# Kernel optimization log

Measured on AMD Instinct MI355X. Metric: run time of the kernel, lower is better.

The kernel has to match this reference:

```python
import jax, jax.numpy as jnp
import numpy as np

N_HEAD = 12
N_EMBD = 768
HEAD_DIM = N_EMBD // N_HEAD


def setup_inputs() -> dict:
    key = jax.random.key(0)
    k1, k2, k3, k4, k5 = jax.random.split(key, 5)
    B, T, C = 1, 4096, N_EMBD
    s = 0.02
    return {
        "x": jax.random.normal(k1, (B, T, C), dtype=jnp.float32),
        "W_qkv": jax.random.normal(k2, (C, 3 * C), dtype=jnp.float32) * s,
        "b_qkv": jnp.zeros((3 * C,), dtype=jnp.float32),
        "W_out": jax.random.normal(k3, (C, C), dtype=jnp.float32) * s,
        "b_out": jnp.zeros((C,), dtype=jnp.float32),
    }


def reference(x, W_qkv, b_qkv, W_out, b_out):
    B, T, C = x.shape
    H, D = N_HEAD, HEAD_DIM
    qkv = x @ W_qkv + b_qkv                       # (B, T, 3C)
    qkv = qkv.reshape(B, T, 3, H, D)
    q = jnp.transpose(qkv[:, :, 0], (0, 2, 1, 3))  # (B, H, T, D)
    k = jnp.transpose(qkv[:, :, 1], (0, 2, 1, 3))
    v = jnp.transpose(qkv[:, :, 2], (0, 2, 1, 3))
    scores = jnp.einsum("bhqd,bhkd->bhqk", q, k) / jnp.sqrt(jnp.float32(D))
    causal = jnp.tril(jnp.ones((T, T), dtype=bool))
    scores = jnp.where(causal[None, None], scores, -jnp.inf)
    weights = jax.nn.softmax(scores, axis=-1)     # (B, H, T, T)
    out = jnp.einsum("bhqk,bhkd->bhqd", weights, v)
    out = jnp.transpose(out, (0, 2, 1, 3)).reshape(B, T, C)
    return out @ W_out + b_out
```

## Files before the change

### kernel.cpp

```cpp
#include <hip/hip_runtime.h>
#include <hip/hip_bf16.h>
#include <stdint.h>

#define T_SEQ 4096
#define C_EMB 768
#define C3    2304
#define CQK   1536
#define NH    12
#define HD    64

typedef __attribute__((ext_vector_type(8))) short short8;
typedef __attribute__((ext_vector_type(4))) short short4v;
typedef __attribute__((ext_vector_type(4))) float f32x4;

__device__ __forceinline__ short f2bf(float f) {
  __bf16 h = (__bf16)f;
  return __builtin_bit_cast(short, h);
}

__device__ __forceinline__ void gload_lds16(const void* g, void* l) {
  __builtin_amdgcn_global_load_lds((const __attribute__((address_space(1))) void*)g,
                                   (__attribute__((address_space(3))) void*)l, 16, 0, 0);
}

__global__ __launch_bounds__(256)
void cvt_kernel(const float* __restrict__ in, short* __restrict__ out, int n4) {
  int i = blockIdx.x * 256 + threadIdx.x;
  if (i < n4) {
    float4 v = ((const float4*)in)[i];
    short4v s = { f2bf(v.x), f2bf(v.y), f2bf(v.z), f2bf(v.w) };
    ((short4v*)out)[i] = s;
  }
}

__global__ __launch_bounds__(256)
void transpose_cvt_kernel(const float* __restrict__ W, short* __restrict__ WT,
                          int K, int N) {
  __shared__ float ts[32][33];
  const int r0 = blockIdx.y * 32, c0 = blockIdx.x * 32;
  const int tid = threadIdx.x;
  {
    int rr = tid >> 3, c4 = (tid & 7) * 4;
    float4 v = *(const float4*)(W + (size_t)(r0 + rr) * N + c0 + c4);
    ts[rr][c4 + 0] = v.x; ts[rr][c4 + 1] = v.y;
    ts[rr][c4 + 2] = v.z; ts[rr][c4 + 3] = v.w;
  }
  __syncthreads();
  {
    int nr = tid >> 3, k4 = (tid & 7) * 4;
    short4v s = { f2bf(ts[k4 + 0][nr]), f2bf(ts[k4 + 1][nr]),
                  f2bf(ts[k4 + 2][nr]), f2bf(ts[k4 + 3][nr]) };
    *(short4v*)(WT + (size_t)(c0 + nr) * K + r0 + k4) = s;
  }
}

template<int BN, bool SPLIT_V, bool OUT_F32>
__global__ __launch_bounds__(256)
void gemm_kernel(const short* __restrict__ A, const short* __restrict__ Bt,
                 const float* __restrict__ bias, void* __restrict__ Cp,
                 short* __restrict__ Vt, int N, int K) {
  constexpr int MF = (BN == 128) ? 4 : 2;
  __shared__ short As[128 * 32];
  __shared__ short Bs[BN * 32];
  const int row0 = blockIdx.y * 128, col0 = blockIdx.x * BN;
  const int tid = threadIdx.x, lane = tid & 63, wave = tid >> 6;
  const int lg = lane >> 4, lr = lane & 15;
  const int wr = (BN == 128) ? ((wave >> 1) * 64) : (wave * 32);
  const int wc = (BN == 128) ? ((wave & 1) * 64) : 0;

  f32x4 acc[MF][4];
  #pragma unroll
  for (int m_ = 0; m_ < MF; ++m_)
    #pragma unroll
    for (int n_ = 0; n_ < 4; ++n_) acc[m_][n_] = (f32x4){0.f, 0.f, 0.f, 0.f};

  const int srow = wave * 16 + (lane >> 2);
  const int scol = (lane & 3) * 8;

  for (int kt = 0; kt < K; kt += 32) {
    __syncthreads();
    #pragma unroll
    for (int c = 0; c < 2; ++c)
      gload_lds16(A + (size_t)(row0 + c * 64 + srow) * K + kt + scol,
                  As + c * 2048 + wave * 512);
    #pragma unroll
    for (int c = 0; c < BN / 64; ++c)
      gload_lds16(Bt + (size_t)(col0 + c * 64 + srow) * K + kt + scol,
                  Bs + c * 2048 + wave * 512);
    __syncthreads();

    short8 a[MF], b[4];
    #pragma unroll
    for (int m_ = 0; m_ < MF; ++m_)
      a[m_] = *(const short8*)&As[(wr + m_ * 16 + lr) * 32 + lg * 8];
    #pragma unroll
    for (int n_ = 0; n_ < 4; ++n_)
      b[n_] = *(const short8*)&Bs[(wc + n_ * 16 + lr) * 32 + lg * 8];
    #pragma unroll
    for (int m_ = 0; m_ < MF; ++m_)
      #pragma unroll
      for (int n_ = 0; n_ < 4; ++n_)
        acc[m_][n_] = __builtin_amdgcn_mfma_f32_16x16x32_bf16(a[m_], b[n_], acc[m_][n_], 0, 0, 0);
  }

  const bool isV = SPLIT_V && (col0 >= CQK);
  #pragma unroll
  for (int n_ = 0; n_ < 4; ++n_) {
    const int col = col0 + wc + n_ * 16 + lr;
    const float bv = bias[col];
    #pragma unroll
    for (int m_ = 0; m_ < MF; ++m_) {
      const int rbase = row0 + wr + m_ * 16 + lg * 4;
      if constexpr (OUT_F32) {
        #pragma unroll
        for (int r = 0; r < 4; ++r)
          ((float*)Cp)[(size_t)(rbase + r) * N + col] = acc[m_][n_][r] + bv;
      } else {
        if (!isV) {
          const int nout = SPLIT_V ? CQK : N;
          #pragma unroll
          for (int r = 0; r < 4; ++r)
            ((short*)Cp)[(size_t)(rbase + r) * nout + col] = f2bf(acc[m_][n_][r] + bv);
        } else {
          short4v p = { f2bf(acc[m_][n_][0] + bv), f2bf(acc[m_][n_][1] + bv),
                        f2bf(acc[m_][n_][2] + bv), f2bf(acc[m_][n_][3] + bv) };
          const int t64 = rbase & 63;
          const int p64 = (t64 & 32) + ((t64 & 12) << 1) + ((t64 & 16) >> 2);
          *(short4v*)(Vt + (size_t)(col - CQK) * T_SEQ + (rbase & ~63) + p64) = p;
        }
      }
    }
  }
}

__global__ __launch_bounds__(512, 4)
void attn_kernel(const short* __restrict__ qk, const short* __restrict__ Vt,
                 short* __restrict__ out) {
  __shared__ short smem[18432];
  const int bd = blockIdx.x;
  const int slot = bd >> 8, c = bd & 255;
  const int j = (slot == 0) ? c : (slot == 1 ? 767 - c : 511 - c);
  const int h = j % NH;
  const int q0 = (63 - j / NH) * 64;
  const int tid = threadIdx.x, lane = tid & 63, wave = tid >> 6;
  const int st = wave >> 2, qslot = wave & 3;
  const int lg = lane >> 4, lr = lane & 15;
  const int q = q0 + qslot * 16 + lr;
  const float SC = 0.18033688011f;

  short (*Ks)[72] = (short(*)[72])(smem + st * 4608);
  short (*Vs)[72] = (short(*)[72])(smem + 9216 + st * 4608);

  short8 qf[2];
  qf[0] = *(const short8*)(qk + (size_t)q * CQK + h * HD + lg * 8);
  qf[1] = *(const short8*)(qk + (size_t)q * CQK + h * HD + 32 + lg * 8);

  float mrun = -1e30f, lrun = 0.f;
  f32x4 o[4];
  #pragma unroll
  for (int d = 0; d < 4; ++d) o[d] = (f32x4){0.f, 0.f, 0.f, 0.f};

  const int srow = qslot * 16 + (lane >> 3);
  const int scol = (lane & 7) * 8;
  const short* Kg = qk + C_EMB + h * HD;
  const short* Vg = Vt + (size_t)(h * HD) * T_SEQ;

  const int ntiles = (q0 >> 6) + 1;
  const int nO = ntiles >> 1, nE = ntiles - nO;
  const int nMine = st ? nO : nE;

  if (nMine > 0) {
    const int kt = st * 64;
    #pragma unroll
    for (int p = 0; p < 2; ++p) {
      const int r = srow + 8 * p;
      *(short8*)&Ks[r][scol] = *(const short8*)(Kg + (size_t)(kt + r) * CQK + scol);
      *(short8*)&Vs[r][scol] = *(const short8*)(Vg + (size_t)r * T_SEQ + kt + scol);
    }
  }
  __syncthreads();

  for (int tt = 0; tt < nE; ++tt) {
    const bool haveNext = (tt + 1 < nMine);
    short8 kr[2], vr[2];
    if (haveNext) {
      const int kt = (2 * (tt + 1) + st) * 64;
      #pragma unroll
      for (int p = 0; p < 2; ++p) {
        const int r = srow + 8 * p;
        kr[p] = *(const short8*)(Kg + (size_t)(kt + r) * CQK + scol);
        vr[p] = *(const short8*)(Vg + (size_t)r * T_SEQ + kt + scol);
      }
    }

    if (tt < nMine) {
      const int tl = 2 * tt + st;
      f32x4 s[4];
      __builtin_amdgcn_s_setprio(1);
      #pragma unroll
      for (int n = 0; n < 4; ++n) {
        f32x4 cc = (f32x4){0.f, 0.f, 0.f, 0.f};
        #pragma unroll
        for (int ks = 0; ks < 2; ++ks) {
          short8 kb = *(const short8*)&Ks[n * 16 + lr][ks * 32 + lg * 8];
          cc = __builtin_amdgcn_mfma_f32_16x16x32_bf16(kb, qf[ks], cc, 0, 0, 0);
        }
        s[n] = cc;
      }
      __builtin_amdgcn_s_setprio(0);

      if (tl == ntiles - 1) {
        #pragma unroll
        for (int n = 0; n < 4; ++n)
          #pragma unroll
          for (int r = 0; r < 4; ++r)
            if (n * 16 + lg * 4 + r > qslot * 16 + lr) s[n][r] = -1e30f;
      }

      float pmax = s[0][0];
      #pragma unroll
      for (int n = 0; n < 4; ++n)
        #pragma unroll
        for (int r = 0; r < 4; ++r) pmax = fmaxf(pmax, s[n][r]);
      pmax = fmaxf(pmax, __shfl_xor(pmax, 16));
      pmax = fmaxf(pmax, __shfl_xor(pmax, 32));

      if (!__all(pmax <= mrun + 44.0f)) {
        const float mn = fmaxf(mrun, pmax);
        const float al = exp2f((mrun - mn) * SC);
        lrun *= al;
        #pragma unroll
        for (int d = 0; d < 4; ++d) o[d] *= al;
        mrun = mn;
      }
      const float msc = mrun * SC;

      float psum = 0.f;
      #pragma unroll
      for (int n = 0; n < 4; ++n)
        #pragma unroll
        for (int r = 0; r < 4; ++r) {
          float p = exp2f(fmaf(s[n][r], SC, -msc));
          s[n][r] = p;
          psum += p;
        }
      psum += __shfl_xor(psum, 16);
      psum += __shfl_xor(psum, 32);
      lrun += psum;

      __builtin_amdgcn_s_setprio(1);
      #pragma unroll
      for (int ks = 0; ks < 2; ++ks) {
        short8 pb = { f2bf(s[2 * ks][0]),     f2bf(s[2 * ks][1]),
                      f2bf(s[2 * ks][2]),     f2bf(s[2 * ks][3]),
                      f2bf(s[2 * ks + 1][0]), f2bf(s[2 * ks + 1][1]),
                      f2bf(s[2 * ks + 1][2]), f2bf(s[2 * ks + 1][3]) };
        #pragma unroll
        for (int d = 0; d < 4; ++d) {
          short8 av = *(const short8*)&Vs[d * 16 + lr][ks * 32 + lg * 8];
          o[d] = __builtin_amdgcn_mfma_f32_16x16x32_bf16(av, pb, o[d], 0, 0, 0);
        }
      }
      __builtin_amdgcn_s_setprio(0);
    }

    __syncthreads();
    if (haveNext) {
      #pragma unroll
      for (int p = 0; p < 2; ++p) {
        const int r = srow + 8 * p;
        *(short8*)&Ks[r][scol] = kr[p];
        *(short8*)&Vs[r][scol] = vr[p];
      }
    }
    __syncthreads();
  }

  float* mo = (float*)smem;
  float* ml = (float*)((char*)smem + 17408);
  if (st == 1) {
    const int row = qslot * 16 + lr;
    #pragma unroll
    for (int d = 0; d < 4; ++d)
      *(f32x4*)&mo[row * 68 + d * 16 + lg * 4] = o[d];
    if (lg == 0) {
      ml[row * 2 + 0] = mrun;
      ml[row * 2 + 1] = lrun;
    }
  }
  __syncthreads();
  if (st == 0) {
    const int row = qslot * 16 + lr;
    const float mb = ml[row * 2 + 0], lb = ml[row * 2 + 1];
    const float M = fmaxf(mrun, mb);
    const float aa = exp2f((mrun - M) * SC);
    const float ab = exp2f((mb - M) * SC);
    const float linv = 1.f / (lrun * aa + lb * ab);
    #pragma unroll
    for (int d = 0; d < 4; ++d) {
      f32x4 ob = *(const f32x4*)&mo[row * 68 + d * 16 + lg * 4];
      short4v ov;
      #pragma unroll
      for (int r = 0; r < 4; ++r)
        ov[r] = f2bf((o[d][r] * aa + ob[r] * ab) * linv);
      *(short4v*)(out + (size_t)q * C_EMB + h * HD + d * 16 + lg * 4) = ov;
    }
  }
}

extern "C" void kernel_launch(void* const* d_in, const int* in_sizes, int n_in,
                              void* d_out, int out_size, void* d_ws, size_t ws_size,
                              hipStream_t stream) {
  const float* x    = (const float*)d_in[0];
  const float* Wqkv = (const float*)d_in[1];
  const float* bqkv = (const float*)d_in[2];
  const float* Wout = (const float*)d_in[3];
  const float* bout = (const float*)d_in[4];

  short* xb    = (short*)d_ws;
  short* WqkvT = xb    + (size_t)T_SEQ * C_EMB;
  short* WoutT = WqkvT + (size_t)C3 * C_EMB;
  short* qk    = WoutT + (size_t)C_EMB * C_EMB;
  short* Vt    = qk    + (size_t)T_SEQ * CQK;

  cvt_kernel<<<(T_SEQ * C_EMB / 4) / 256, 256, 0, stream>>>(x, xb, T_SEQ * C_EMB / 4);
  transpose_cvt_kernel<<<dim3(C3 / 32, C_EMB / 32), 256, 0, stream>>>(Wqkv, WqkvT, C_EMB, C3);
  transpose_cvt_kernel<<<dim3(C_EMB / 32, C_EMB / 32), 256, 0, stream>>>(Wout, WoutT, C_EMB, C_EMB);

  gemm_kernel<128, true, false><<<dim3(C3 / 128, T_SEQ / 128), 256, 0, stream>>>(
      xb, WqkvT, bqkv, qk, Vt, C3, C_EMB);

  attn_kernel<<<dim3(768), 512, 0, stream>>>(qk, Vt, xb);

  gemm_kernel<64, false, true><<<dim3(C_EMB / 64, T_SEQ / 128), 256, 0, stream>>>(
      xb, WoutT, bout, d_out, nullptr, C_EMB, C_EMB);
}
```

Before: 132.1 us.

## Split causal attention KV range into chunks with a separate merge kernel

Replaces the one-block-per-query-tile causal attention schedule with a split-KV scheme. Each query tile's key range is cut into chunks of 16 tiles, and long tiles get up to 4 blocks, for 1920 blocks in place of 768. Partial outputs and running max/sum go to fp32 workspace and a new merge kernel combines them. This balances load and shortens the critical path of the long query tiles. It costs an extra launch and extra global traffic for the partials.

```diff
diff --git a/kernel.cpp b/kernel.cpp
--- a/kernel.cpp
+++ b/kernel.cpp
@@ -8,6 +8,8 @@
 #define CQK   1536
 #define NH    12
 #define HD    64
+#define CH    16
+#define NSLOT 1728
 
 typedef __attribute__((ext_vector_type(8))) short short8;
 typedef __attribute__((ext_vector_type(4))) short short4v;
@@ -135,13 +137,23 @@
 
 __global__ __launch_bounds__(512, 4)
 void attn_kernel(const short* __restrict__ qk, const short* __restrict__ Vt,
-                 short* __restrict__ out) {
+                 short* __restrict__ out, float* __restrict__ pO,
+                 float* __restrict__ pML) {
   __shared__ short smem[18432];
   const int bd = blockIdx.x;
-  const int slot = bd >> 8, c = bd & 255;
-  const int j = (slot == 0) ? c : (slot == 1 ? 767 - c : 511 - c);
-  const int h = j % NH;
-  const int q0 = (63 - j / NH) * 64;
+  const int h = bd % NH;
+  const int ii = 159 - bd / NH;
+  int qt, ck;
+  if (ii < 16)      { qt = ii;                 ck = 0; }
+  else if (ii < 48) { qt = 16 + (ii - 16) / 2; ck = (ii - 16) % 2; }
+  else if (ii < 96) { qt = 32 + (ii - 48) / 3; ck = (ii - 48) % 3; }
+  else              { qt = 48 + (ii - 96) / 4; ck = (ii - 96) % 4; }
+  const int q0 = qt * 64;
+  const int ntiles = qt + 1;
+  const int t0 = ck * CH;
+  const int rem = ntiles - t0;
+  const int nloc = rem < CH ? rem : CH;
+
   const int tid = threadIdx.x, lane = tid & 63, wave = tid >> 6;
   const int st = wave >> 2, qslot = wave & 3;
   const int lg = lane >> 4, lr = lane & 15;
@@ -165,12 +177,11 @@
   const short* Kg = qk + C_EMB + h * HD;
   const short* Vg = Vt + (size_t)(h * HD) * T_SEQ;
 
-  const int ntiles = (q0 >> 6) + 1;
-  const int nO = ntiles >> 1, nE = ntiles - nO;
+  const int nO = nloc >> 1, nE = nloc - nO;
   const int nMine = st ? nO : nE;
 
   if (nMine > 0) {
-    const int kt = st * 64;
+    const int kt = (t0 + st) * 64;
     #pragma unroll
     for (int p = 0; p < 2; ++p) {
       const int r = srow + 8 * p;
@@ -184,7 +195,7 @@
     const bool haveNext = (tt + 1 < nMine);
     short8 kr[2], vr[2];
     if (haveNext) {
-      const int kt = (2 * (tt + 1) + st) * 64;
+      const int kt = (t0 + 2 * (tt + 1) + st) * 64;
       #pragma unroll
       for (int p = 0; p < 2; ++p) {
         const int r = srow + 8 * p;
@@ -194,7 +205,7 @@
     }
 
     if (tt < nMine) {
-      const int tl = 2 * tt + st;
+      const int tl = t0 + 2 * tt + st;
       f32x4 s[4];
       __builtin_amdgcn_s_setprio(1);
       #pragma unroll
@@ -295,16 +306,90 @@
     const float M = fmaxf(mrun, mb);
     const float aa = exp2f((mrun - M) * SC);
     const float ab = exp2f((mb - M) * SC);
-    const float linv = 1.f / (lrun * aa + lb * ab);
-    #pragma unroll
-    for (int d = 0; d < 4; ++d) {
-      f32x4 ob = *(const f32x4*)&mo[row * 68 + d * 16 + lg * 4];
-      short4v ov;
-      #pragma unroll
-      for (int r = 0; r < 4; ++r)
-        ov[r] = f2bf((o[d][r] * aa + ob[r] * ab) * linv);
-      *(short4v*)(out + (size_t)q * C_EMB + h * HD + d * 16 + lg * 4) = ov;
-    }
+    const float lmerged = lrun * aa + lb * ab;
+    if (qt < CH) {
+      const float linv = 1.f / lmerged;
+      #pragma unroll
+      for (int d = 0; d < 4; ++d) {
+        f32x4 ob = *(const f32x4*)&mo[row * 68 + d * 16 + lg * 4];
+        short4v ov;
+        #pragma unroll
+        for (int r = 0; r < 4; ++r)
+          ov[r] = f2bf((o[d][r] * aa + ob[r] * ab) * linv);
+        *(short4v*)(out + (size_t)q * C_EMB + h * HD + d * 16 + lg * 4) = ov;
+      }
+    } else {
+      const int sbase = (qt < 32) ? 2 * (qt - 16)
+                      : (qt < 48) ? 32 + 3 * (qt - 32)
+                                  : 80 + 4 * (qt - 48);
+      const int slot = h * 144 + sbase + ck;
+      float* po = pO + (size_t)slot * 4096 + row * 64;
+      #pragma unroll
+      for (int d = 0; d < 4; ++d) {
+        f32x4 ob = *(const f32x4*)&mo[row * 68 + d * 16 + lg * 4];
+        f32x4 v;
+        #pragma unroll
+        for (int r = 0; r < 4; ++r) v[r] = o[d][r] * aa + ob[r] * ab;
+        *(f32x4*)&po[d * 16 + lg * 4] = v;
+      }
+      if (lg == 0) {
+        pML[(size_t)slot * 128 + row * 2 + 0] = M;
+        pML[(size_t)slot * 128 + row * 2 + 1] = lmerged;
+      }
+    }
+  }
+}
+
+__global__ __launch_bounds__(256)
+void merge_kernel(const float* __restrict__ pO, const float* __restrict__ pML,
+                  short* __restrict__ out) {
+  const int bd = blockIdx.x;
+  const int h = bd % NH;
+  const int qt = 16 + bd / NH;
+  const int nc = qt / CH + 1;
+  const int sbase = (qt < 32) ? 2 * (qt - 16)
+                  : (qt < 48) ? 32 + 3 * (qt - 32)
+                              : 80 + 4 * (qt - 48);
+  const int slot0 = h * 144 + sbase;
+  const int tid = threadIdx.x;
+  const int q = tid >> 2, dc = (tid & 3) << 4;
+  const float SC = 0.18033688011f;
+
+  float mi[4], li[4];
+  float M = -1e30f;
+  #pragma unroll
+  for (int i = 0; i < 4; ++i)
+    if (i < nc) {
+      mi[i] = pML[(size_t)(slot0 + i) * 128 + q * 2 + 0];
+      li[i] = pML[(size_t)(slot0 + i) * 128 + q * 2 + 1];
+      M = fmaxf(M, mi[i]);
+    }
+
+  f32x4 O[4];
+  #pragma unroll
+  for (int d4 = 0; d4 < 4; ++d4) O[d4] = (f32x4){0.f, 0.f, 0.f, 0.f};
+  float L = 0.f;
+  #pragma unroll
+  for (int i = 0; i < 4; ++i)
+    if (i < nc) {
+      const float a = exp2f((mi[i] - M) * SC);
+      L = fmaf(li[i], a, L);
+      const float* po = pO + (size_t)(slot0 + i) * 4096 + q * 64 + dc;
+      #pragma unroll
+      for (int d4 = 0; d4 < 4; ++d4) {
+        f32x4 v = *(const f32x4*)(po + d4 * 4);
+        #pragma unroll
+        for (int r = 0; r < 4; ++r) O[d4][r] = fmaf(v[r], a, O[d4][r]);
+      }
+    }
+
+  const float linv = 1.f / L;
+  #pragma unroll
+  for (int d4 = 0; d4 < 4; ++d4) {
+    short4v ov;
+    #pragma unroll
+    for (int r = 0; r < 4; ++r) ov[r] = f2bf(O[d4][r] * linv);
+    *(short4v*)(out + (size_t)(qt * 64 + q) * C_EMB + h * HD + dc + d4 * 4) = ov;
   }
 }
 
@@ -322,6 +407,8 @@
   short* WoutT = WqkvT + (size_t)C3 * C_EMB;
   short* qk    = WoutT + (size_t)C_EMB * C_EMB;
   short* Vt    = qk    + (size_t)T_SEQ * CQK;
+  float* pO    = (float*)(Vt + (size_t)C_EMB * T_SEQ);
+  float* pML   = pO + (size_t)NSLOT * 4096;
 
   cvt_kernel<<<(T_SEQ * C_EMB / 4) / 256, 256, 0, stream>>>(x, xb, T_SEQ * C_EMB / 4);
   transpose_cvt_kernel<<<dim3(C3 / 32, C_EMB / 32), 256, 0, stream>>>(Wqkv, WqkvT, C_EMB, C3);
@@ -330,7 +417,8 @@
   gemm_kernel<128, true, false><<<dim3(C3 / 128, T_SEQ / 128), 256, 0, stream>>>(
       xb, WqkvT, bqkv, qk, Vt, C3, C_EMB);
 
-  attn_kernel<<<dim3(768), 512, 0, stream>>>(qk, Vt, xb);
+  attn_kernel<<<dim3(NH * 160), 512, 0, stream>>>(qk, Vt, xb, pO, pML);
+  merge_kernel<<<dim3(NH * 48), 256, 0, stream>>>(pO, pML, xb);
 
   gemm_kernel<64, false, true><<<dim3(C_EMB / 64, T_SEQ / 128), 256, 0, stream>>>(
       xb, WoutT, bout, d_out, nullptr, C_EMB, C_EMB);
```

Result: slower. 140.7 us (+6.5%).
